# Performance work log

Measured on AMD Instinct MI355X. Metric: run time of the kernel, lower is better.

## Reference

```python
import jax, jax.numpy as jnp
import numpy as np

N_NODES = 100000
FEAT = 256
MAX_DEG = 128
BATCH = 1024
# sampler k uses layer_infos[num_layers-1-k].num_samples: layer_infos num_samples = [25, 10]
NUM_SAMPLES_PER_HOP = [10, 25]
DEPTH = 2


def setup_inputs() -> dict:
    key = jax.random.key(0)
    ks = jax.random.split(key, 10)
    s = 0.05
    return {
        "features": jax.random.normal(ks[0], (N_NODES, FEAT), jnp.float32),
        "w_self_0": jax.random.normal(ks[3], (FEAT, 128), jnp.float32) * s,
        "w_neigh_0": jax.random.normal(ks[4], (FEAT, 128), jnp.float32) * s,
        "w_self_1": jax.random.normal(ks[5], (256, 128), jnp.float32) * s,  # in = 2*128 concat
        "w_neigh_1": jax.random.normal(ks[6], (256, 128), jnp.float32) * s,
        "w_out": jax.random.normal(ks[7], (256, 1), jnp.float32) * s,
        "b_out": jnp.zeros((1,), jnp.float32),
        "node_ids": jax.random.randint(ks[2], (BATCH,), 0, N_NODES, jnp.int32),
        "adj": jax.random.randint(ks[1], (N_NODES, MAX_DEG), 0, N_NODES, jnp.int32),
    }


def _sample(node_ids, adj):
    """Multi-hop uniform neighbor sampling (UniformNeighborSampler chain)."""
    skey = jax.random.key(42)
    samples = [node_ids.reshape(-1)]
    for k, ns in enumerate(NUM_SAMPLES_PER_HOP):
        ids = samples[k]
        rows = jnp.take(adj, ids, axis=0)  # [M, MAX_DEG]
        cols = jax.random.randint(jax.random.fold_in(skey, k), (ids.shape[0], ns), 0, adj.shape[1])
        samples.append(jnp.take_along_axis(rows, cols, axis=1).reshape(-1))
    return samples


def reference(features, w_self_0, w_neigh_0, w_self_1, w_neigh_1, w_out, b_out, node_ids, adj):
    samples = _sample(node_ids, adj)
    hidden = [jnp.take(features, s, axis=0) for s in samples]
    params = [(w_self_0, w_neigh_0), (w_self_1, w_neigh_1)]
    for k in range(DEPTH):
        w_s, w_n = params[k]
        next_hidden = []
        for hop in range(DEPTH - k):
            self_v = hidden[hop]                                   # [M, d]
            neigh = hidden[hop + 1].reshape(self_v.shape[0], NUM_SAMPLES_PER_HOP[hop], -1)
            neigh_mean = neigh.mean(axis=1)                        # [M, d]
            # MeanAggregator, concat=True: relu(concat(self@Ws, mean@Wn))
            next_hidden.append(jax.nn.relu(jnp.concatenate([self_v @ w_s, neigh_mean @ w_n], axis=1)))
        hidden = next_hidden
    h = hidden[0]                                                  # [BATCH, 256]
    h = h / jnp.sqrt(jnp.maximum(jnp.sum(h * h, axis=1, keepdims=True), 1e-12))  # l2_normalize
    return h @ w_out + b_out                                       # Dense(1)
```

## Files before the change

### kernel.cpp

```cpp
#include <hip/hip_runtime.h>
#include <math.h>

struct K2 { unsigned a, b; };

__host__ __device__ constexpr unsigned rotl32c(unsigned x, int r) {
  return (x << r) | (x >> (32 - r));
}

__host__ __device__ constexpr K2 threefry2x32(unsigned k0, unsigned k1,
                                              unsigned x0, unsigned x1) {
  const unsigned ks2 = k0 ^ k1 ^ 0x1BD11BDAu;
  const unsigned ks[3] = {k0, k1, ks2};
  const int rotA[4] = {13, 15, 26, 6};
  const int rotB[4] = {17, 29, 16, 24};
  x0 += k0; x1 += k1;
  for (int g = 0; g < 5; ++g) {
    const int* rr = (g & 1) ? rotB : rotA;
    for (int i = 0; i < 4; ++i) {
      x0 += x1;
      x1 = rotl32c(x1, rr[i]);
      x1 ^= x0;
    }
    x0 += ks[(g + 1) % 3];
    x1 += ks[(g + 2) % 3] + (unsigned)(g + 1);
  }
  return K2{x0, x1};
}

__host__ __device__ constexpr K2 hop_key(unsigned k) {
  K2 f = threefry2x32(0u, 42u, 0u, k);
  return threefry2x32(f.a, f.b, 0u, 1u);
}

constexpr K2 HK0 = hop_key(0u);
constexpr K2 HK1 = hop_key(1u);

__global__ __launch_bounds__(256) void sample_means(
    const int* __restrict__ node_ids, const int* __restrict__ adj,
    const float* __restrict__ feat, int* __restrict__ s1,
    float* __restrict__ nm1, float* __restrict__ nm0) {
  const int blk = blockIdx.x;
  const int w = threadIdx.x >> 6;
  const int lane = threadIdx.x & 63;

  if (blk < 2560) {
    const int m = blk * 4 + w;
    K2 r0 = threefry2x32(HK0.a, HK0.b, 0u, (unsigned)m);
    const int nid = adj[(long long)node_ids[m / 10] * 128 +
                        (int)((r0.a ^ r0.b) & 127u)];
    if (lane == 0) s1[m] = nid;
    int srow;
    {
      unsigned i = (unsigned)(m * 25 + (lane < 25 ? lane : 0));
      K2 r = threefry2x32(HK1.a, HK1.b, 0u, i);
      srow = adj[(long long)nid * 128 + (int)((r.a ^ r.b) & 127u)];
    }
    float4 acc = make_float4(0.f, 0.f, 0.f, 0.f);
#pragma unroll
    for (int c = 0; c < 25; c += 5) {
      float4 v[5];
#pragma unroll
      for (int j = 0; j < 5; ++j) {
        long long row = (long long)__shfl(srow, c + j, 64);
        v[j] = *(const float4*)(feat + row * 256 + (lane << 2));
      }
#pragma unroll
      for (int j = 0; j < 5; ++j) {
        acc.x += v[j].x; acc.y += v[j].y; acc.z += v[j].z; acc.w += v[j].w;
      }
    }
    const float s = 1.f / 25.f;
    acc.x *= s; acc.y *= s; acc.z *= s; acc.w *= s;
    *(float4*)(nm1 + (long long)m * 256 + (lane << 2)) = acc;
  } else {
    const int m0 = (blk - 2560) * 4 + w;
    int srow;
    {
      int j = lane < 10 ? lane : 0;
      K2 r = threefry2x32(HK0.a, HK0.b, 0u, (unsigned)(m0 * 10 + j));
      srow = adj[(long long)node_ids[m0] * 128 + (int)((r.a ^ r.b) & 127u)];
    }
    float4 acc = make_float4(0.f, 0.f, 0.f, 0.f);
#pragma unroll
    for (int c = 0; c < 10; c += 5) {
      float4 v[5];
#pragma unroll
      for (int j = 0; j < 5; ++j) {
        long long row = (long long)__shfl(srow, c + j, 64);
        v[j] = *(const float4*)(feat + row * 256 + (lane << 2));
      }
#pragma unroll
      for (int j = 0; j < 5; ++j) {
        acc.x += v[j].x; acc.y += v[j].y; acc.z += v[j].z; acc.w += v[j].w;
      }
    }
    acc.x *= 0.1f; acc.y *= 0.1f; acc.z *= 0.1f; acc.w *= 0.1f;
    *(float4*)(nm0 + (long long)m0 * 256 + (lane << 2)) = acc;
  }
}

struct GemmCfg {
  const float* A; const int* idx; const float* B; float* C;
  int ccol0; int mtiles; int tiles;
};
struct GemmCfg4 { GemmCfg c[4]; };

__global__ __launch_bounds__(256) void gemm_relu_multi(GemmCfg4 cfgs) {
  int b = blockIdx.x, z = 0;
  while (z < 3 && b >= cfgs.c[z].tiles) { b -= cfgs.c[z].tiles; ++z; }
  const GemmCfg cfg = cfgs.c[z];
  const int mt = b % cfg.mtiles;
  const int nt = b / cfg.mtiles;

  __shared__ __align__(16) float As[16][68];
  __shared__ __align__(16) float Bs[16][68];

  const int t = threadIdx.x;
  const int tx = t & 15, ty = t >> 4;

  const int arow = t >> 2;
  const int ak4 = (t & 3) << 2;
  const int grow = mt * 64 + arow;
  const long long asrc = cfg.idx ? (long long)cfg.idx[grow] : (long long)grow;
  const float* Ap = cfg.A + asrc * 256 + ak4;

  const int bkk = t >> 4;
  const int bn4 = (t & 15) << 2;
  const float* Bp = cfg.B + bkk * 128 + nt * 64 + bn4;

  float acc[4][4] = {};

  for (int k0 = 0; k0 < 256; k0 += 16) {
    float4 av = *(const float4*)(Ap + k0);
    float4 bv = *(const float4*)(Bp + (long long)k0 * 128);
    __syncthreads();
    As[ak4 + 0][arow] = av.x;
    As[ak4 + 1][arow] = av.y;
    As[ak4 + 2][arow] = av.z;
    As[ak4 + 3][arow] = av.w;
    *(float4*)&Bs[bkk][bn4] = bv;
    __syncthreads();
#pragma unroll
    for (int kk = 0; kk < 16; ++kk) {
      float4 a = *(const float4*)&As[kk][ty << 2];
      float4 b4 = *(const float4*)&Bs[kk][tx << 2];
      acc[0][0] += a.x * b4.x; acc[0][1] += a.x * b4.y; acc[0][2] += a.x * b4.z; acc[0][3] += a.x * b4.w;
      acc[1][0] += a.y * b4.x; acc[1][1] += a.y * b4.y; acc[1][2] += a.y * b4.z; acc[1][3] += a.y * b4.w;
      acc[2][0] += a.z * b4.x; acc[2][1] += a.z * b4.y; acc[2][2] += a.z * b4.z; acc[2][3] += a.z * b4.w;
      acc[3][0] += a.w * b4.x; acc[3][1] += a.w * b4.y; acc[3][2] += a.w * b4.z; acc[3][3] += a.w * b4.w;
    }
  }

#pragma unroll
  for (int i = 0; i < 4; ++i) {
    const int r = mt * 64 + (ty << 2) + i;
    float* Cp = cfg.C + (long long)r * 256 + cfg.ccol0 + nt * 64 + (tx << 2);
#pragma unroll
    for (int j = 0; j < 4; ++j) {
      float v = acc[i][j];
      Cp[j] = v > 0.f ? v : 0.f;
    }
  }
}

template <int S>
__global__ __launch_bounds__(256) void mean_rows_w(
    const float* __restrict__ src, float* __restrict__ dst, float invS) {
  const int m = blockIdx.x * 4 + (threadIdx.x >> 6);
  const int lane = threadIdx.x & 63;
  const long long base = (long long)m * S;

  float4 acc = make_float4(0.f, 0.f, 0.f, 0.f);
#pragma unroll
  for (int c = 0; c < S; c += 5) {
    float4 v[5];
#pragma unroll
    for (int j = 0; j < 5; ++j)
      v[j] = *(const float4*)(src + (base + c + j) * 256 + (lane << 2));
#pragma unroll
    for (int j = 0; j < 5; ++j) {
      acc.x += v[j].x; acc.y += v[j].y; acc.z += v[j].z; acc.w += v[j].w;
    }
  }
  acc.x *= invS; acc.y *= invS; acc.z *= invS; acc.w *= invS;
  *(float4*)(dst + (long long)m * 256 + (lane << 2)) = acc;
}

__global__ __launch_bounds__(256) void layer1_final(
    const float* __restrict__ out0, const float* __restrict__ nml1,
    const float* __restrict__ ws1, const float* __restrict__ wn1,
    const float* __restrict__ w_out, const float* __restrict__ b_out,
    float* __restrict__ out) {
  __shared__ __align__(16) float As[16][520];
  __shared__ __align__(16) float Bs[16][260];
  __shared__ __align__(16) float Hs[16][260];

  const int t = threadIdx.x;
  const int r0 = blockIdx.x * 16;

#pragma unroll
  for (int i = 0; i < 8; ++i) {
    const int f = t + (i << 8);
    const int row = f >> 7, c4 = f & 127;
    const float* src = (c4 < 64)
        ? out0 + (long long)(r0 + row) * 256 + (c4 << 2)
        : nml1 + (long long)(r0 + row) * 256 + ((c4 - 64) << 2);
    *(float4*)&As[row][c4 << 2] = *(const float4*)src;
  }

  const int m = t >> 4;
  const int cb = t & 15;
  const int aoff = (cb < 8) ? 0 : 256;

  const int skk = t >> 4;
  const int sc = (t & 15) << 4;
  const float* bbase = (sc < 128) ? ws1 + sc : wn1 + (sc - 128);

  float acc[16] = {};

  for (int k0 = 0; k0 < 256; k0 += 16) {
    const float* bsrc = bbase + (k0 + skk) * 128;
    __syncthreads();
#pragma unroll
    for (int u = 0; u < 4; ++u)
      *(float4*)&Bs[skk][sc + (u << 2)] = *(const float4*)(bsrc + (u << 2));
    __syncthreads();
#pragma unroll
    for (int q = 0; q < 16; ++q) {
      const float a = As[m][aoff + k0 + q];
#pragma unroll
      for (int j4 = 0; j4 < 4; ++j4) {
        float4 b4 = *(const float4*)&Bs[q][(cb << 4) + (j4 << 2)];
        acc[j4 * 4 + 0] += a * b4.x;
        acc[j4 * 4 + 1] += a * b4.y;
        acc[j4 * 4 + 2] += a * b4.z;
        acc[j4 * 4 + 3] += a * b4.w;
      }
    }
  }

#pragma unroll
  for (int j4 = 0; j4 < 4; ++j4) {
    float4 h4;
    h4.x = fmaxf(acc[j4 * 4 + 0], 0.f);
    h4.y = fmaxf(acc[j4 * 4 + 1], 0.f);
    h4.z = fmaxf(acc[j4 * 4 + 2], 0.f);
    h4.w = fmaxf(acc[j4 * 4 + 3], 0.f);
    *(float4*)&Hs[m][(cb << 4) + (j4 << 2)] = h4;
  }
  __syncthreads();

  const int wv = t >> 6, lane = t & 63;
  for (int rr = 0; rr < 4; ++rr) {
    const int row = wv * 4 + rr;
    float4 h4 = *(const float4*)&Hs[row][lane << 2];
    float4 w4 = *(const float4*)&w_out[lane << 2];
    float ss = h4.x * h4.x + h4.y * h4.y + h4.z * h4.z + h4.w * h4.w;
    float dd = h4.x * w4.x + h4.y * w4.y + h4.z * w4.z + h4.w * w4.w;
    for (int off = 32; off; off >>= 1) {
      ss += __shfl_down(ss, off, 64);
      dd += __shfl_down(dd, off, 64);
    }
    if (lane == 0)
      out[r0 + row] = dd / sqrtf(fmaxf(ss, 1e-12f)) + b_out[0];
  }
}

extern "C" void kernel_launch(void* const* d_in, const int* in_sizes, int n_in,
                              void* d_out, int out_size, void* d_ws, size_t ws_size,
                              hipStream_t stream) {
  (void)in_sizes; (void)n_in; (void)out_size; (void)ws_size;

  const float* features  = (const float*)d_in[0];
  const float* w_self_0  = (const float*)d_in[1];
  const float* w_neigh_0 = (const float*)d_in[2];
  const float* w_self_1  = (const float*)d_in[3];
  const float* w_neigh_1 = (const float*)d_in[4];
  const float* w_out     = (const float*)d_in[5];
  const float* b_out     = (const float*)d_in[6];
  const int*   node_ids  = (const int*)d_in[7];
  const int*   adj       = (const int*)d_in[8];
  float* out = (float*)d_out;

  char* ws = (char*)d_ws;
  size_t off = 0;
  auto alloc = [&](size_t bytes) -> void* {
    void* p = ws + off;
    off = (off + bytes + 255) & ~(size_t)255;
    return p;
  };
  int*   s1   = (int*)alloc(10240 * sizeof(int));
  float* nm1  = (float*)alloc((size_t)10240 * 256 * 4);
  float* nm0  = (float*)alloc((size_t)1024 * 256 * 4);
  float* out1 = (float*)alloc((size_t)10240 * 256 * 4);
  float* out0 = (float*)alloc((size_t)1024 * 256 * 4);
  float* nml1 = (float*)alloc((size_t)1024 * 256 * 4);

  sample_means<<<2816, 256, 0, stream>>>(node_ids, adj, features, s1, nm1, nm0);

  {
    GemmCfg4 cf;
    cf.c[0] = {features, s1,       w_self_0,  out1, 0,   160, 320};
    cf.c[1] = {nm1,      nullptr,  w_neigh_0, out1, 128, 160, 320};
    cf.c[2] = {features, node_ids, w_self_0,  out0, 0,   16,  32};
    cf.c[3] = {nm0,      nullptr,  w_neigh_0, out0, 128, 16,  32};
    gemm_relu_multi<<<704, 256, 0, stream>>>(cf);
  }

  mean_rows_w<10><<<256, 256, 0, stream>>>(out1, nml1, 0.1f);

  layer1_final<<<64, 256, 0, stream>>>(out0, nml1, w_self_1, w_neigh_1,
                                       w_out, b_out, out);
}
```

Measured before the change: 268.6 us.

## Split hop-1 sampling, prefetch GEMM tiles, fuse mean into final layer

Hop-1 neighbor sampling moves into a small separate kernel, so sample_means reads s1 instead of recomputing threefry per wave, and the hop-0 mean path reuses s1. The GEMM loop now prefetches the next A/B tile into registers before the inner product to overlap global loads with compute. The mean_rows kernel is fused into the final layer kernel, which removes one launch and the nml1 round trip. This adds one extra tiny launch and puts the 10-row mean reads inside only 64 blocks, which may serialise those reads.

```diff
diff --git a/kernel.cpp b/kernel.cpp
--- a/kernel.cpp
+++ b/kernel.cpp
@@ -35,20 +35,27 @@
 constexpr K2 HK0 = hop_key(0u);
 constexpr K2 HK1 = hop_key(1u);
 
+__global__ __launch_bounds__(256) void sample_hop1(
+    const int* __restrict__ ids, const int* __restrict__ adj,
+    int* __restrict__ out, int n) {
+  int i = blockIdx.x * 256 + threadIdx.x;
+  if (i >= n) return;
+  K2 r = threefry2x32(HK0.a, HK0.b, 0u, (unsigned)i);
+  int col = (int)((r.a ^ r.b) & 127u);
+  out[i] = adj[(long long)ids[i / 10] * 128 + col];
+}
+
 __global__ __launch_bounds__(256) void sample_means(
-    const int* __restrict__ node_ids, const int* __restrict__ adj,
-    const float* __restrict__ feat, int* __restrict__ s1,
-    float* __restrict__ nm1, float* __restrict__ nm0) {
+    const int* __restrict__ s1, const int* __restrict__ adj,
+    const float* __restrict__ feat, float* __restrict__ nm1,
+    float* __restrict__ nm0) {
   const int blk = blockIdx.x;
   const int w = threadIdx.x >> 6;
   const int lane = threadIdx.x & 63;
 
   if (blk < 2560) {
     const int m = blk * 4 + w;
-    K2 r0 = threefry2x32(HK0.a, HK0.b, 0u, (unsigned)m);
-    const int nid = adj[(long long)node_ids[m / 10] * 128 +
-                        (int)((r0.a ^ r0.b) & 127u)];
-    if (lane == 0) s1[m] = nid;
+    const int nid = s1[m];
     int srow;
     {
       unsigned i = (unsigned)(m * 25 + (lane < 25 ? lane : 0));
@@ -74,12 +81,7 @@
     *(float4*)(nm1 + (long long)m * 256 + (lane << 2)) = acc;
   } else {
     const int m0 = (blk - 2560) * 4 + w;
-    int srow;
-    {
-      int j = lane < 10 ? lane : 0;
-      K2 r = threefry2x32(HK0.a, HK0.b, 0u, (unsigned)(m0 * 10 + j));
-      srow = adj[(long long)node_ids[m0] * 128 + (int)((r.a ^ r.b) & 127u)];
-    }
+    const int srow = s1[(long long)m0 * 10 + (lane < 10 ? lane : 0)];
     float4 acc = make_float4(0.f, 0.f, 0.f, 0.f);
 #pragma unroll
     for (int c = 0; c < 10; c += 5) {
@@ -128,11 +130,11 @@
   const int bn4 = (t & 15) << 2;
   const float* Bp = cfg.B + bkk * 128 + nt * 64 + bn4;
 
+  float4 av = *(const float4*)Ap;
+  float4 bv = *(const float4*)Bp;
   float acc[4][4] = {};
 
   for (int k0 = 0; k0 < 256; k0 += 16) {
-    float4 av = *(const float4*)(Ap + k0);
-    float4 bv = *(const float4*)(Bp + (long long)k0 * 128);
     __syncthreads();
     As[ak4 + 0][arow] = av.x;
     As[ak4 + 1][arow] = av.y;
@@ -140,6 +142,10 @@
     As[ak4 + 3][arow] = av.w;
     *(float4*)&Bs[bkk][bn4] = bv;
     __syncthreads();
+    if (k0 + 16 < 256) {
+      av = *(const float4*)(Ap + k0 + 16);
+      bv = *(const float4*)(Bp + (long long)(k0 + 16) * 128);
+    }
 #pragma unroll
     for (int kk = 0; kk < 16; ++kk) {
       float4 a = *(const float4*)&As[kk][ty << 2];
@@ -163,31 +169,8 @@
   }
 }
 
-template <int S>
-__global__ __launch_bounds__(256) void mean_rows_w(
-    const float* __restrict__ src, float* __restrict__ dst, float invS) {
-  const int m = blockIdx.x * 4 + (threadIdx.x >> 6);
-  const int lane = threadIdx.x & 63;
-  const long long base = (long long)m * S;
-
-  float4 acc = make_float4(0.f, 0.f, 0.f, 0.f);
-#pragma unroll
-  for (int c = 0; c < S; c += 5) {
-    float4 v[5];
-#pragma unroll
-    for (int j = 0; j < 5; ++j)
-      v[j] = *(const float4*)(src + (base + c + j) * 256 + (lane << 2));
-#pragma unroll
-    for (int j = 0; j < 5; ++j) {
-      acc.x += v[j].x; acc.y += v[j].y; acc.z += v[j].z; acc.w += v[j].w;
-    }
-  }
-  acc.x *= invS; acc.y *= invS; acc.z *= invS; acc.w *= invS;
-  *(float4*)(dst + (long long)m * 256 + (lane << 2)) = acc;
-}
-
-__global__ __launch_bounds__(256) void layer1_final(
-    const float* __restrict__ out0, const float* __restrict__ nml1,
+__global__ __launch_bounds__(256) void tail_fused(
+    const float* __restrict__ out0, const float* __restrict__ out1,
     const float* __restrict__ ws1, const float* __restrict__ wn1,
     const float* __restrict__ w_out, const float* __restrict__ b_out,
     float* __restrict__ out) {
@@ -197,15 +180,33 @@
 
   const int t = threadIdx.x;
   const int r0 = blockIdx.x * 16;
-
-#pragma unroll
-  for (int i = 0; i < 8; ++i) {
+  const int wv = t >> 6, lane = t & 63;
+
+#pragma unroll
+  for (int i = 0; i < 4; ++i) {
     const int f = t + (i << 8);
-    const int row = f >> 7, c4 = f & 127;
-    const float* src = (c4 < 64)
-        ? out0 + (long long)(r0 + row) * 256 + (c4 << 2)
-        : nml1 + (long long)(r0 + row) * 256 + ((c4 - 64) << 2);
-    *(float4*)&As[row][c4 << 2] = *(const float4*)src;
+    const int row = f >> 6, c4 = f & 63;
+    *(float4*)&As[row][c4 << 2] =
+        *(const float4*)(out0 + (long long)(r0 + row) * 256 + (c4 << 2));
+  }
+#pragma unroll
+  for (int rr = 0; rr < 4; ++rr) {
+    const int row = (wv << 2) + rr;
+    const long long base = (long long)(r0 + row) * 10;
+    float4 acc = make_float4(0.f, 0.f, 0.f, 0.f);
+#pragma unroll
+    for (int c = 0; c < 10; c += 5) {
+      float4 v[5];
+#pragma unroll
+      for (int j = 0; j < 5; ++j)
+        v[j] = *(const float4*)(out1 + (base + c + j) * 256 + (lane << 2));
+#pragma unroll
+      for (int j = 0; j < 5; ++j) {
+        acc.x += v[j].x; acc.y += v[j].y; acc.z += v[j].z; acc.w += v[j].w;
+      }
+    }
+    acc.x *= 0.1f; acc.y *= 0.1f; acc.z *= 0.1f; acc.w *= 0.1f;
+    *(float4*)&As[row][256 + (lane << 2)] = acc;
   }
 
   const int m = t >> 4;
@@ -250,9 +251,8 @@
   }
   __syncthreads();
 
-  const int wv = t >> 6, lane = t & 63;
   for (int rr = 0; rr < 4; ++rr) {
-    const int row = wv * 4 + rr;
+    const int row = (wv << 2) + rr;
     float4 h4 = *(const float4*)&Hs[row][lane << 2];
     float4 w4 = *(const float4*)&w_out[lane << 2];
     float ss = h4.x * h4.x + h4.y * h4.y + h4.z * h4.z + h4.w * h4.w;
@@ -294,9 +294,10 @@
   float* nm0  = (float*)alloc((size_t)1024 * 256 * 4);
   float* out1 = (float*)alloc((size_t)10240 * 256 * 4);
   float* out0 = (float*)alloc((size_t)1024 * 256 * 4);
-  float* nml1 = (float*)alloc((size_t)1024 * 256 * 4);
-
-  sample_means<<<2816, 256, 0, stream>>>(node_ids, adj, features, s1, nm1, nm0);
+
+  sample_hop1<<<40, 256, 0, stream>>>(node_ids, adj, s1, 10240);
+
+  sample_means<<<2816, 256, 0, stream>>>(s1, adj, features, nm1, nm0);
 
   {
     GemmCfg4 cf;
@@ -307,8 +308,6 @@
     gemm_relu_multi<<<704, 256, 0, stream>>>(cf);
   }
 
-  mean_rows_w<10><<<256, 256, 0, stream>>>(out1, nml1, 0.1f);
-
-  layer1_final<<<64, 256, 0, stream>>>(out0, nml1, w_self_1, w_neigh_1,
-                                       w_out, b_out, out);
-}
+  tail_fused<<<64, 256, 0, stream>>>(out0, out1, w_self_1, w_neigh_1,
+                                     w_out, b_out, out);
+}
```

New measurement: 269.0 us. About the same (+0.1%).
